# Optimization experiments

Hardware: AMD Instinct MI355X
Metric: run time of the kernel (lower is better)

The kernel has to match this reference:

```python
import jax, jax.numpy as jnp
import numpy as np

N, E, MUL, ATTR, NBASIS = 30000, 480000, 32, 8, 8
AVG_NEIGH = 16.0
INV_SQRT3 = 1.0 / np.sqrt(3.0).astype(np.float32)  # wigner 3j (1,1,0)
LOG2 = float(np.log(2.0))


def ssp(x):
    # shifted softplus: softplus(x) - log(2)
    return jax.nn.softplus(x) - LOG2


def setup_inputs() -> dict:
    key = jax.random.key(0)
    ks = jax.random.split(key, 15)
    return {
        "node_s": jax.random.normal(ks[0], (N, MUL), jnp.float32),
        "node_v": jax.random.normal(ks[1], (N, MUL, 3), jnp.float32),
        "node_attr": jax.random.uniform(ks[2], (N, ATTR), jnp.float32),
        "edge_attr": jax.random.normal(ks[3], (E, 4), jnp.float32),       # [sh0 | sh1(3)]
        "edge_scalars": jax.random.uniform(ks[4], (E, NBASIS), jnp.float32),
        "W1_0": jax.random.normal(ks[5], (MUL, MUL), jnp.float32),
        "W1_1": jax.random.normal(ks[6], (MUL, MUL), jnp.float32),
        "Wfc1": jax.random.normal(ks[7], (NBASIS, NBASIS), jnp.float32),
        "Wfc2": jax.random.normal(ks[8], (NBASIS, 4 * MUL), jnp.float32),
        "W2_0": jax.random.normal(ks[9], (2 * MUL, MUL), jnp.float32),
        "W2_1": jax.random.normal(ks[10], (2 * MUL, MUL), jnp.float32),
        "Wsc0": jax.random.normal(ks[11], (MUL, ATTR, MUL), jnp.float32),
        "Wsc1": jax.random.normal(ks[12], (MUL, ATTR, MUL), jnp.float32),
        "edge_src": jax.random.randint(ks[13], (E,), 0, N, jnp.int32),
        "edge_dst": jax.random.randint(ks[14], (E,), 0, N, jnp.int32),
    }


def reference(node_s, node_v, node_attr, edge_attr, edge_scalars,
              W1_0, W1_1, Wfc1, Wfc2, W2_0, W2_1, Wsc0, Wsc1,
              edge_src, edge_dst):
    n_nodes, mul = node_s.shape
    # --- fc: radial MLP -> per-edge TP weights (shared_weights=False) ---
    h = ssp(edge_scalars @ Wfc1 * (1.0 / np.sqrt(Wfc1.shape[0])))
    w = h @ Wfc2 * (1.0 / np.sqrt(Wfc2.shape[0]))                 # [E, 4*MUL]
    w00, w01, w10, w11 = jnp.split(w, 4, axis=1)                  # instruction order
    # --- lin1: per-irrep linear (fan-in normalized) ---
    inv_m = 1.0 / np.sqrt(mul)
    x0 = node_s @ W1_0 * inv_m                                    # [N, MUL]
    x1 = jnp.einsum('nud,uw->nwd', node_v, W1_1) * inv_m          # [N, MUL, 3]
    # --- gather destination-node features per edge ---
    x0d, x1d = x0[edge_dst], x1[edge_dst]
    sh0, sh1 = edge_attr[:, :1], edge_attr[:, 1:4]
    # --- uvu tensor product with per-edge weights ---
    s_a = w00 * x0d * sh0                                         # 0e x 0e -> 0e
    s_b = w11 * jnp.einsum('eud,ed->eu', x1d, sh1) * INV_SQRT3    # 1o x 1o -> 0e
    v_a = (w01 * x0d)[:, :, None] * sh1[:, None, :]               # 0e x 1o -> 1o
    v_b = w10[:, :, None] * x1d * sh0[:, :, None]                 # 1o x 0e -> 1o
    mid_s = jnp.concatenate([s_a, s_b], axis=1)                   # [E, 64]  (64x0e)
    mid_v = jnp.concatenate([v_a, v_b], axis=1)                   # [E, 64, 3] (64x1o)
    # --- scatter-sum over edge_src, normalized by sqrt(avg_num_neighbors) ---
    inv_nb = 1.0 / np.sqrt(AVG_NEIGH)
    agg_s = jax.ops.segment_sum(mid_s, edge_src, num_segments=n_nodes) * inv_nb
    agg_v = jax.ops.segment_sum(mid_v, edge_src, num_segments=n_nodes) * inv_nb
    # --- lin2 ---
    inv_2m = 1.0 / np.sqrt(2.0 * mul)
    out0 = agg_s @ W2_0 * inv_2m                                  # [N, MUL]
    out1 = jnp.einsum('nud,uw->nwd', agg_v, W2_1) * inv_2m        # [N, MUL, 3]
    # --- self-connection: fully-connected TP (attr is scalar 8x0e) ---
    sc_norm = 1.0 / np.sqrt(mul * node_attr.shape[1])
    sc0 = jnp.einsum('nu,nv,uvw->nw', node_s, node_attr, Wsc0) * sc_norm
    sc1 = jnp.einsum('nud,nv,uvw->nwd', node_v, node_attr, Wsc1) * sc_norm
    o0 = out0 + sc0
    o1 = out1 + sc1
    return jnp.concatenate([o0, o1.reshape(n_nodes, mul * 3)], axis=1)  # [N, 128]
```

## Files before the change

### kernel.cpp

```cpp
#include <hip/hip_runtime.h>
#include <math.h>

#define N_NODES 30000
#define N_EDGES 480000

typedef __attribute__((ext_vector_type(8))) short short8;
typedef __attribute__((ext_vector_type(4))) float f32x4;
typedef __attribute__((ext_vector_type(2))) float f32x2;

__device__ __forceinline__ unsigned short f2bf(float f) {
    unsigned u = __float_as_uint(f);
    u += 0x7fff + ((u >> 16) & 1);
    return (unsigned short)(u >> 16);
}
__device__ __forceinline__ float bfLO(unsigned v) { return __uint_as_float(v << 16); }
__device__ __forceinline__ float bfHI(unsigned v) { return __uint_as_float(v & 0xffff0000u); }
__device__ __forceinline__ unsigned packbf(float a, float b) {
    return (unsigned)f2bf(a) | ((unsigned)f2bf(b) << 16);
}
__device__ __forceinline__ unsigned ptk(float a, float b) {
    return (__float_as_uint(a) >> 16) | (__float_as_uint(b) & 0xffff0000u);
}

union U8 { short8 v; unsigned u[4]; };
union C4 { f32x4 v; float f[4]; };

__global__ __launch_bounds__(256) void k_pre(
    const float* __restrict__ node_s,
    const float* __restrict__ node_v,
    const float* __restrict__ W1_0,
    const float* __restrict__ W1_1,
    const float* __restrict__ Wsc0,
    const float* __restrict__ Wsc1,
    const float* __restrict__ W2_0,
    const float* __restrict__ W2_1,
    const int* __restrict__ edge_src,
    int* __restrict__ deg,
    unsigned short* __restrict__ xnode,
    unsigned* __restrict__ bsc0,
    unsigned* __restrict__ bsc1,
    unsigned* __restrict__ b20,
    unsigned* __restrict__ b21)
{
    __shared__ float sVT[16 * 100];
    __shared__ float sXo[16 * 140];
    int tid = threadIdx.x;

    if (blockIdx.x >= 1875) {
        int b = blockIdx.x - 1875;
        const float* Wm = (b == 0) ? Wsc0 : (b == 1) ? Wsc1 : (b == 2) ? W2_0 : W2_1;
        unsigned* dst = (b == 0) ? bsc0 : (b == 1) ? bsc1 : (b == 2) ? b20 : b21;
        float scale = (b < 2) ? 0.0625f : 0.03125f;
        int nu = (b < 2) ? 4096 : 1024;
        for (int idx = tid; idx < nu; idx += 256) {
            int jp = idx & 3;
            int lane = (idx >> 2) & 63;
            int ft = (idx >> 8) & 1;
            int kc = idx >> 9;
            int quad = lane >> 4, col = lane & 15;
            int k = kc * 32 + quad * 8 + jp * 2;
            int c = ft * 16 + col;
            dst[idx] = packbf(Wm[k * 32 + c] * scale, Wm[(k + 1) * 32 + c] * scale);
        }
        return;
    }

    atomicAdd(&deg[edge_src[blockIdx.x * 256 + tid]], 1);

    int nbase = blockIdx.x * 16;
    for (int i = tid; i < 1536; i += 256) {
        int nl = i / 96, r = i - nl * 96;
        int u = r / 3, d = r - u * 3;
        sVT[nl * 100 + d * 32 + u] = node_v[(size_t)nbase * 96 + i];
    }
    __syncthreads();

    int lane = tid & 63;
    int wv = tid >> 6;
    int col = lane & 15, quad = lane >> 4, m = lane & 15;

    const float* W1 = (wv == 0) ? W1_0 : W1_1;
    U8 bf0, bf1;
#pragma unroll
    for (int p = 0; p < 4; ++p) {
        int k = quad * 8 + 2 * p;
        bf0.u[p] = packbf(W1[k * 32 + col],      W1[(k + 1) * 32 + col]);
        bf1.u[p] = packbf(W1[k * 32 + col + 16], W1[(k + 1) * 32 + col + 16]);
    }

    U8 af;
    if (wv == 0) {
        const float* sp = node_s + (size_t)(nbase + m) * 32 + quad * 8;
        float4 a0 = *(const float4*)(sp);
        float4 a1 = *(const float4*)(sp + 4);
        af.u[0] = packbf(a0.x, a0.y); af.u[1] = packbf(a0.z, a0.w);
        af.u[2] = packbf(a1.x, a1.y); af.u[3] = packbf(a1.z, a1.w);
    } else {
        int R = 16 * (wv - 1) + m;
        int nl = R / 3, d = R - nl * 3;
        const float* vp = sVT + nl * 100 + d * 32 + quad * 8;
        af.u[0] = packbf(vp[0], vp[1]); af.u[1] = packbf(vp[2], vp[3]);
        af.u[2] = packbf(vp[4], vp[5]); af.u[3] = packbf(vp[6], vp[7]);
    }

    f32x4 acc0 = {0.f, 0.f, 0.f, 0.f};
    f32x4 acc1 = {0.f, 0.f, 0.f, 0.f};
    acc0 = __builtin_amdgcn_mfma_f32_16x16x32_bf16(af.v, bf0.v, acc0, 0, 0, 0);
    acc1 = __builtin_amdgcn_mfma_f32_16x16x32_bf16(af.v, bf1.v, acc1, 0, 0, 0);

    C4 c0, c1;
    c0.v = acc0; c1.v = acc1;
    if (wv == 0) {
#pragma unroll
        for (int r = 0; r < 4; ++r) {
            int nl = (quad << 2) + r;
            sXo[nl * 140 + col]      = c0.f[r];
            sXo[nl * 140 + col + 16] = c1.f[r];
        }
    } else {
#pragma unroll
        for (int r = 0; r < 4; ++r) {
            int R = 16 * (wv - 1) + (quad << 2) + r;
            int nl = R / 3, d = R - nl * 3;
            sXo[nl * 140 + (1 + d) * 34 + col]      = c0.f[r];
            sXo[nl * 140 + (1 + d) * 34 + col + 16] = c1.f[r];
        }
    }
    __syncthreads();

    const float inv_m = 0.1767766953f;
    for (int i = tid; i < 512; i += 256) {
        int nl = i >> 5, u = i & 31;
        const float* xp = sXo + nl * 140;
        uint2 pk;
        pk.x = packbf(xp[u] * inv_m,       xp[34 + u] * inv_m);
        pk.y = packbf(xp[68 + u] * inv_m,  xp[102 + u] * inv_m);
        *(uint2*)(xnode + (size_t)(nbase + nl) * 128 + u * 4) = pk;
    }
}

__global__ __launch_bounds__(1024) void scan_kernel(const int* __restrict__ deg,
                                                    int* __restrict__ offs,
                                                    int* __restrict__ cursor) {
    __shared__ int sdeg[N_NODES];
    __shared__ int wsum[16];
    int tid = threadIdx.x;
#pragma unroll
    for (int k = 0; k < 30; ++k) {
        int idx = k * 1024 + tid;
        if (idx < N_NODES) sdeg[idx] = deg[idx];
    }
    __syncthreads();
    int base = tid * 30;
    int s = 0;
    if (base < N_NODES) {
#pragma unroll
        for (int k = 0; k < 30; ++k) s += sdeg[base + k];
    }
    int lane = tid & 63, wid = tid >> 6;
    int inc = s;
#pragma unroll
    for (int d = 1; d < 64; d <<= 1) {
        int o = __shfl_up(inc, d, 64);
        if (lane >= d) inc += o;
    }
    if (lane == 63) wsum[wid] = inc;
    __syncthreads();
    if (tid < 16) {
        int v = wsum[tid];
        int t = v;
#pragma unroll
        for (int d = 1; d < 16; d <<= 1) {
            int o = __shfl_up(t, d, 64);
            if (tid >= d) t += o;
        }
        wsum[tid] = t - v;
    }
    __syncthreads();
    int run = inc - s + wsum[wid];
    if (base < N_NODES) {
#pragma unroll
        for (int k = 0; k < 30; ++k) {
            int n = base + k;
            int d = sdeg[n];
            sdeg[n] = run;
            run += d;
        }
    }
    __syncthreads();
#pragma unroll
    for (int k = 0; k < 30; ++k) {
        int idx = k * 1024 + tid;
        if (idx < N_NODES) {
            int v = sdeg[idx];
            offs[idx] = v;
            cursor[idx] = v;
        }
    }
    if (tid == 0) offs[N_NODES] = N_EDGES;
}

__global__ __launch_bounds__(256) void fill_kernel(
    const float* __restrict__ edge_attr,
    const float* __restrict__ edge_scalars,
    const float* __restrict__ Wfc1,
    const int* __restrict__ edge_src,
    const int* __restrict__ edge_dst,
    int* __restrict__ cursor,
    uint4* __restrict__ rec)
{
    __shared__ float sW[64];
    int tid = threadIdx.x;
    if (tid < 64) sW[tid] = Wfc1[tid];
    __syncthreads();

    int e = blockIdx.x * 256 + tid;
    float4 es0 = *(const float4*)(edge_scalars + (size_t)e * 8);
    float4 es1 = *(const float4*)(edge_scalars + (size_t)e * 8 + 4);
    float4 ea  = *(const float4*)(edge_attr + (size_t)e * 4);
    int src = edge_src[e];
    int dst = edge_dst[e];
    int pos = atomicAdd(&cursor[src], 1);

    const float inv8 = 0.3535533906f;
    float h[8];
#pragma unroll
    for (int i = 0; i < 8; ++i) {
        float acc = es0.x * sW[0 * 8 + i];
        acc = fmaf(es0.y, sW[1 * 8 + i], acc);
        acc = fmaf(es0.z, sW[2 * 8 + i], acc);
        acc = fmaf(es0.w, sW[3 * 8 + i], acc);
        acc = fmaf(es1.x, sW[4 * 8 + i], acc);
        acc = fmaf(es1.y, sW[5 * 8 + i], acc);
        acc = fmaf(es1.z, sW[6 * 8 + i], acc);
        acc = fmaf(es1.w, sW[7 * 8 + i], acc);
        acc *= inv8;
        float ax = fabsf(acc);
        float tt = __expf(-ax);
        h[i] = fmaxf(acc, 0.f) + __logf(1.f + tt) - 0.6931471806f;
    }
    uint4 r0, r1;
    r0.x = packbf(h[0], h[1]); r0.y = packbf(h[2], h[3]);
    r0.z = packbf(h[4], h[5]); r0.w = packbf(h[6], h[7]);
    r1.x = packbf(ea.x, ea.y); r1.y = packbf(ea.z, ea.w);
    r1.z = ((unsigned)dst) << 8;
    r1.w = 0;
    rec[2 * pos]     = r0;
    rec[2 * pos + 1] = r1;
}

struct GAcc {
    float sa, sb, va2, vb2;
    f32x2 va01, vb01;
};

__device__ __forceinline__ void gstep(
    uint4& RS0, uint4& RS1, uint2& XS, const uint4& RN1, uint2& XN,
    int& t, int cntH, int& pf, int L,
    const char* recc, const char* xbc,
    const f32x2* wfA, const f32x2* wfB, GAcc& g)
{
    float hv[8];
    hv[0] = bfLO(RS0.x); hv[1] = bfHI(RS0.x);
    hv[2] = bfLO(RS0.y); hv[3] = bfHI(RS0.y);
    hv[4] = bfLO(RS0.z); hv[5] = bfHI(RS0.z);
    hv[6] = bfLO(RS0.w); hv[7] = bfHI(RS0.w);
    float sh0  = bfLO(RS1.x), s1xe = bfHI(RS1.x);
    float s1ye = bfLO(RS1.y), s1ze = bfHI(RS1.y);
    float xv0 = bfLO(XS.x), xd0 = bfHI(XS.x);
    float xd1 = bfLO(XS.y), xd2 = bfHI(XS.y);
    bool ok = (t < cntH);

    RS0 = *(const uint4*)(recc + pf);
    RS1 = *(const uint4*)(recc + pf + 16);
    pf = min(pf + 64, L);
    XN = *(const uint2*)(xbc + RN1.z);

    f32x2 aA = {0.f, 0.f}, aB = {0.f, 0.f};
#pragma unroll
    for (int q = 0; q < 8; ++q) {
        f32x2 hh = {hv[q], hv[q]};
        aA = __builtin_elementwise_fma(hh, wfA[q], aA);
        aB = __builtin_elementwise_fma(hh, wfB[q], aB);
    }
    float a00 = ok ? aA.x : 0.f;
    float a01 = ok ? aA.y : 0.f;
    float a10 = ok ? aB.x : 0.f;
    float a11 = ok ? aB.y : 0.f;

    float dot = xd0 * s1xe + xd1 * s1ye + xd2 * s1ze;
    g.sa = fmaf(a00 * sh0, xv0, g.sa);
    g.sb = fmaf(a11, dot, g.sb);
    float w01x0 = a01 * xv0;
    float t10 = a10 * sh0;
    f32x2 wb = {w01x0, w01x0};
    f32x2 tb = {t10, t10};
    f32x2 s01 = {s1xe, s1ye};
    f32x2 xd01 = {xd0, xd1};
    g.va01 = __builtin_elementwise_fma(wb, s01, g.va01);
    g.vb01 = __builtin_elementwise_fma(tb, xd01, g.vb01);
    g.va2 = fmaf(w01x0, s1ze, g.va2);
    g.vb2 = fmaf(t10, xd2, g.vb2);
    ++t;
}

__global__ __launch_bounds__(256) void k_main(
    const int* __restrict__ offs,
    const uint4* __restrict__ rec,
    const float* __restrict__ Wfc2,
    const unsigned short* __restrict__ xnode,
    const float* __restrict__ node_s,
    const float* __restrict__ node_v,
    const float* __restrict__ node_attr,
    const unsigned* __restrict__ bsc0,
    const unsigned* __restrict__ bsc1,
    const unsigned* __restrict__ b20,
    const unsigned* __restrict__ b21,
    float* __restrict__ out)
{
    __shared__ float sWf[1024];
    __shared__ float sS[16 * 33];
    __shared__ float sV[16 * 100];
    __shared__ unsigned short sAgg[16 * 264];
    int tid = threadIdx.x;

    const float inv8 = 0.3535533906f;
    const float inv_s3 = 0.5773502692f;
    for (int i = tid; i < 1024; i += 256) {
        float sc = ((i & 127) >= 96) ? inv8 * inv_s3 : inv8;
        sWf[i] = Wfc2[i] * sc;
    }
    int nbase = blockIdx.x * 16;
    for (int i = tid; i < 512; i += 256)
        sS[(i >> 5) * 33 + (i & 31)] = node_s[(size_t)nbase * 32 + i];
    for (int i = tid; i < 1536; i += 256)
        sV[(i / 96) * 100 + (i % 96)] = node_v[(size_t)nbase * 96 + i];
    __syncthreads();

    int lane = tid & 63;
    int u = lane & 31;
    int half = lane >> 5;
    int wv = tid >> 6;

    f32x2 wfA[8], wfB[8];
#pragma unroll
    for (int q = 0; q < 8; ++q) {
        const float* wp = sWf + q * 128 + u;
        wfA[q].x = wp[0];  wfA[q].y = wp[32];
        wfB[q].x = wp[64]; wfB[q].y = wp[96];
    }

    int nfirst = nbase + wv * 4;
    int beg = offs[nfirst];
#pragma unroll 1
    for (int j = 0; j < 4; ++j) {
        int end = offs[nfirst + j + 1];
        int cnt = end - beg;

        GAcc g;
        g.sa = 0.f; g.sb = 0.f; g.va2 = 0.f; g.vb2 = 0.f;
        g.va01 = (f32x2){0.f, 0.f};
        g.vb01 = (f32x2){0.f, 0.f};

        if (cnt > 0) {
            const char* recc = (const char*)rec;
            const char* xbc  = (const char*)xnode + u * 8;
            int T = (cnt + 1) >> 1;
            int cntH = (cnt + 1 - half) >> 1;
            int L = (end - 1) * 32;
            int b0 = (beg + half) * 32;

            uint4 r00, r01, r10, r11, r20, r21, r30, r31, r40, r41, r50, r51;
            uint2 x0, x1, x2, x3, x4, x5;
            x4.x = 0u; x4.y = 0u; x5.x = 0u; x5.y = 0u;
            int p;
            p = min(b0,       L); r00 = *(const uint4*)(recc + p); r01 = *(const uint4*)(recc + p + 16);
            p = min(b0 + 64,  L); r10 = *(const uint4*)(recc + p); r11 = *(const uint4*)(recc + p + 16);
            p = min(b0 + 128, L); r20 = *(const uint4*)(recc + p); r21 = *(const uint4*)(recc + p + 16);
            p = min(b0 + 192, L); r30 = *(const uint4*)(recc + p); r31 = *(const uint4*)(recc + p + 16);
            p = min(b0 + 256, L); r40 = *(const uint4*)(recc + p); r41 = *(const uint4*)(recc + p + 16);
            p = min(b0 + 320, L); r50 = *(const uint4*)(recc + p); r51 = *(const uint4*)(recc + p + 16);
            int pf = min(b0 + 384, L);
            x0 = *(const uint2*)(xbc + r01.z);
            x1 = *(const uint2*)(xbc + r11.z);
            x2 = *(const uint2*)(xbc + r21.z);
            x3 = *(const uint2*)(xbc + r31.z);

            int t = 0;
            int Tm = T - 5;
            while (t < Tm) {
                gstep(r00, r01, x0, r41, x4, t, cntH, pf, L, recc, xbc, wfA, wfB, g);
                gstep(r10, r11, x1, r51, x5, t, cntH, pf, L, recc, xbc, wfA, wfB, g);
                gstep(r20, r21, x2, r01, x0, t, cntH, pf, L, recc, xbc, wfA, wfB, g);
                gstep(r30, r31, x3, r11, x1, t, cntH, pf, L, recc, xbc, wfA, wfB, g);
                gstep(r40, r41, x4, r21, x2, t, cntH, pf, L, recc, xbc, wfA, wfB, g);
                gstep(r50, r51, x5, r31, x3, t, cntH, pf, L, recc, xbc, wfA, wfB, g);
            }
            if (t < T) gstep(r00, r01, x0, r41, x4, t, cntH, pf, L, recc, xbc, wfA, wfB, g);
            if (t < T) gstep(r10, r11, x1, r51, x5, t, cntH, pf, L, recc, xbc, wfA, wfB, g);
            if (t < T) gstep(r20, r21, x2, r01, x0, t, cntH, pf, L, recc, xbc, wfA, wfB, g);
            if (t < T) gstep(r30, r31, x3, r11, x1, t, cntH, pf, L, recc, xbc, wfA, wfB, g);
            if (t < T) gstep(r40, r41, x4, r21, x2, t, cntH, pf, L, recc, xbc, wfA, wfB, g);
        }

        g.sa      += __shfl_xor(g.sa, 32, 64);
        g.sb      += __shfl_xor(g.sb, 32, 64);
        g.va01.x  += __shfl_xor(g.va01.x, 32, 64);
        g.va01.y  += __shfl_xor(g.va01.y, 32, 64);
        g.vb01.x  += __shfl_xor(g.vb01.x, 32, 64);
        g.vb01.y  += __shfl_xor(g.vb01.y, 32, 64);
        g.va2     += __shfl_xor(g.va2, 32, 64);
        g.vb2     += __shfl_xor(g.vb2, 32, 64);

        int nl = wv * 4 + j;
        unsigned short* ap = sAgg + nl * 264;
        if (half == 0) {
            ap[u]       = f2bf(g.sa);
            ap[32 + u]  = f2bf(g.sb);
            ap[64 + u]  = f2bf(g.va01.x);
            ap[96 + u]  = f2bf(g.vb01.x);
        } else {
            ap[128 + u] = f2bf(g.va01.y);
            ap[160 + u] = f2bf(g.vb01.y);
            ap[192 + u] = f2bf(g.va2);
            ap[224 + u] = f2bf(g.vb2);
        }
        beg = end;
    }
    __syncthreads();

    int col = lane & 15;
    int quad = lane >> 4;
    int m = col;
    bool is_s = (wv == 0);
    int sub = wv - 1;

    const short* Bs = (const short*)(is_s ? bsc0 : bsc1);
    const short* B2 = (const short*)(is_s ? b20 : b21);

    int aBase, fbase, fstep, n_a;
    if (is_s) {
        aBase = m * 264;
        fbase = m * 33;
        fstep = 1;
        n_a = nbase + m;
    } else {
        int r16 = 16 * sub + m;
        int nl = r16 / 3;
        int dd = r16 - nl * 3;
        aBase = nl * 264 + 64 + 64 * dd;
        fbase = nl * 100 + dd;
        fstep = 3;
        n_a = nbase + nl;
    }
    float4 A0 = *(const float4*)(node_attr + (size_t)n_a * 8);
    float4 A1 = *(const float4*)(node_attr + (size_t)n_a * 8 + 4);
    float aa0 = A0.x, aa1 = A0.y, aa2 = A0.z, aa3 = A0.w;
    float aa4 = A1.x, aa5 = A1.y, aa6 = A1.z, aa7 = A1.w;

    f32x4 acc0 = {0.f, 0.f, 0.f, 0.f};
    f32x4 acc1 = {0.f, 0.f, 0.f, 0.f};

#pragma unroll
    for (int kc = 0; kc < 2; ++kc) {
        short8 af = *(const short8*)((const short*)sAgg + aBase + kc * 32 + quad * 8);
        short8 bf0 = *(const short8*)(B2 + ((kc * 2 + 0) * 64 + lane) * 8);
        short8 bf1 = *(const short8*)(B2 + ((kc * 2 + 1) * 64 + lane) * 8);
        acc0 = __builtin_amdgcn_mfma_f32_16x16x32_bf16(af, bf0, acc0, 0, 0, 0);
        acc1 = __builtin_amdgcn_mfma_f32_16x16x32_bf16(af, bf1, acc1, 0, 0, 0);
    }
    const float* Sf = is_s ? sS : sV;
#pragma unroll
    for (int kc = 0; kc < 8; ++kc) {
        int uu = kc * 4 + quad;
        float f = Sf[fbase + uu * fstep];
        U8 af;
        af.u[0] = ptk(f * aa0, f * aa1);
        af.u[1] = ptk(f * aa2, f * aa3);
        af.u[2] = ptk(f * aa4, f * aa5);
        af.u[3] = ptk(f * aa6, f * aa7);
        short8 bf0 = *(const short8*)(Bs + ((kc * 2 + 0) * 64 + lane) * 8);
        short8 bf1 = *(const short8*)(Bs + ((kc * 2 + 1) * 64 + lane) * 8);
        acc0 = __builtin_amdgcn_mfma_f32_16x16x32_bf16(af.v, bf0, acc0, 0, 0, 0);
        acc1 = __builtin_amdgcn_mfma_f32_16x16x32_bf16(af.v, bf1, acc1, 0, 0, 0);
    }

    C4 c0, c1;
    c0.v = acc0; c1.v = acc1;
    if (is_s) {
#pragma unroll
        for (int r = 0; r < 4; ++r) {
            int n = nbase + (quad << 2) + r;
            out[(size_t)n * 128 + col]      = c0.f[r];
            out[(size_t)n * 128 + col + 16] = c1.f[r];
        }
    } else {
#pragma unroll
        for (int r = 0; r < 4; ++r) {
            int rl = 16 * sub + (quad << 2) + r;
            int nn = rl / 3;
            int dd = rl - nn * 3;
            int n = nbase + nn;
            out[(size_t)n * 128 + 32 + 3 * col + dd]        = c0.f[r];
            out[(size_t)n * 128 + 32 + 3 * (col + 16) + dd] = c1.f[r];
        }
    }
}

extern "C" void kernel_launch(void* const* d_in, const int* in_sizes, int n_in,
                              void* d_out, int out_size, void* d_ws, size_t ws_size,
                              hipStream_t stream) {
    const float* node_s       = (const float*)d_in[0];
    const float* node_v       = (const float*)d_in[1];
    const float* node_attr    = (const float*)d_in[2];
    const float* edge_attr    = (const float*)d_in[3];
    const float* edge_scalars = (const float*)d_in[4];
    const float* W1_0 = (const float*)d_in[5];
    const float* W1_1 = (const float*)d_in[6];
    const float* Wfc1 = (const float*)d_in[7];
    const float* Wfc2 = (const float*)d_in[8];
    const float* W2_0 = (const float*)d_in[9];
    const float* W2_1 = (const float*)d_in[10];
    const float* Wsc0 = (const float*)d_in[11];
    const float* Wsc1 = (const float*)d_in[12];
    const int* edge_src = (const int*)d_in[13];
    const int* edge_dst = (const int*)d_in[14];

    char* ws = (char*)d_ws;
    unsigned short* xnode = (unsigned short*)(ws);
    uint4* rec            = (uint4*)(ws + 7680000);
    int* deg    = (int*)(ws + 23040000);
    int* offs   = (int*)(ws + 23160000);
    int* cursor = (int*)(ws + 23280016);
    unsigned* bsc0 = (unsigned*)(ws + 23400064);
    unsigned* bsc1 = (unsigned*)(ws + 23416448);
    unsigned* b20  = (unsigned*)(ws + 23432832);
    unsigned* b21  = (unsigned*)(ws + 23436928);

    hipMemsetAsync(deg, 0, (size_t)N_NODES * sizeof(int), stream);
    k_pre<<<1879, 256, 0, stream>>>(node_s, node_v, W1_0, W1_1, Wsc0, Wsc1,
                                    W2_0, W2_1, edge_src, deg, xnode,
                                    bsc0, bsc1, b20, b21);
    scan_kernel<<<1, 1024, 0, stream>>>(deg, offs, cursor);
    fill_kernel<<<1875, 256, 0, stream>>>(edge_attr, edge_scalars, Wfc1,
                                          edge_src, edge_dst, cursor, rec);
    k_main<<<1875, 256, 0, stream>>>(offs, rec, Wfc2, xnode,
                                     node_s, node_v, node_attr,
                                     bsc0, bsc1, b20, b21, (float*)d_out);
}
```

Before: 230.2 us.

## Record per-edge slot in counting pass and fold scan into preprocessing kernel

A new counting kernel stores each edge's atomic return value, so the fill kernel computes its position as offs[src]+epos instead of issuing a second atomic. The single-block scan kernel is removed, and block 0 of k_pre now performs a chunked prefix scan that runs alongside the node transforms. k_main reads Wfc2 straight into registers instead of staging it through shared memory, which drops a barrier. In exchange this adds one launch, uses the output buffer as scratch for epos, and makes block 0 of k_pre a serial scan that may become the critical path.

```diff
diff --git a/kernel.cpp b/kernel.cpp
--- a/kernel.cpp
+++ b/kernel.cpp
@@ -24,6 +24,15 @@
 
 union U8 { short8 v; unsigned u[4]; };
 union C4 { f32x4 v; float f[4]; };
+
+__global__ __launch_bounds__(256) void k_count(
+    const int* __restrict__ edge_src,
+    int* __restrict__ deg,
+    int* __restrict__ epos)
+{
+    int e = blockIdx.x * 256 + threadIdx.x;
+    epos[e] = atomicAdd(&deg[edge_src[e]], 1);
+}
 
 __global__ __launch_bounds__(256) void k_pre(
     const float* __restrict__ node_s,
@@ -34,20 +43,69 @@
     const float* __restrict__ Wsc1,
     const float* __restrict__ W2_0,
     const float* __restrict__ W2_1,
-    const int* __restrict__ edge_src,
-    int* __restrict__ deg,
+    const int* __restrict__ deg,
+    int* __restrict__ offs,
     unsigned short* __restrict__ xnode,
     unsigned* __restrict__ bsc0,
     unsigned* __restrict__ bsc1,
     unsigned* __restrict__ b20,
     unsigned* __restrict__ b21)
 {
-    __shared__ float sVT[16 * 100];
-    __shared__ float sXo[16 * 140];
+    __shared__ __align__(16) char smem[15360];
+    __shared__ int wsb[6];
+    float* sVT = (float*)smem;
+    float* sXo = (float*)(smem + 6400);
+    int*   sdg = (int*)smem;
     int tid = threadIdx.x;
 
-    if (blockIdx.x >= 1875) {
-        int b = blockIdx.x - 1875;
+    if (blockIdx.x == 0) {
+        int lane = tid & 63, wid = tid >> 6;
+        int running = 0;
+        for (int c = 0; c < N_NODES; c += 3840) {
+            int size = min(3840, N_NODES - c);
+#pragma unroll
+            for (int k = 0; k < 15; ++k) {
+                int i = tid + k * 256;
+                sdg[i] = (i < size) ? deg[c + i] : 0;
+            }
+            __syncthreads();
+            int bt = tid * 15;
+            int s = 0;
+#pragma unroll
+            for (int k = 0; k < 15; ++k) s += sdg[bt + k];
+            int inc = s;
+#pragma unroll
+            for (int d = 1; d < 64; d <<= 1) {
+                int o = __shfl_up(inc, d, 64);
+                if (lane >= d) inc += o;
+            }
+            if (lane == 63) wsb[wid] = inc;
+            __syncthreads();
+            if (tid == 0) {
+                int t0 = 0;
+#pragma unroll
+                for (int w = 0; w < 4; ++w) { int v = wsb[w]; wsb[w] = t0; t0 += v; }
+                wsb[4] = t0;
+            }
+            __syncthreads();
+            int run2 = inc - s + wsb[wid] + running;
+#pragma unroll
+            for (int k = 0; k < 15; ++k) {
+                int idx = bt + k;
+                int gi = c + idx;
+                int d = sdg[idx];
+                if (gi < N_NODES) offs[gi] = run2;
+                run2 += d;
+            }
+            running += wsb[4];
+            __syncthreads();
+        }
+        if (tid == 0) offs[N_NODES] = N_EDGES;
+        return;
+    }
+
+    if (blockIdx.x >= 1876) {
+        int b = blockIdx.x - 1876;
         const float* Wm = (b == 0) ? Wsc0 : (b == 1) ? Wsc1 : (b == 2) ? W2_0 : W2_1;
         unsigned* dst = (b == 0) ? bsc0 : (b == 1) ? bsc1 : (b == 2) ? b20 : b21;
         float scale = (b < 2) ? 0.0625f : 0.03125f;
@@ -65,9 +123,7 @@
         return;
     }
 
-    atomicAdd(&deg[edge_src[blockIdx.x * 256 + tid]], 1);
-
-    int nbase = blockIdx.x * 16;
+    int nbase = (blockIdx.x - 1) * 16;
     for (int i = tid; i < 1536; i += 256) {
         int nl = i / 96, r = i - nl * 96;
         int u = r / 3, d = r - u * 3;
@@ -139,74 +195,14 @@
     }
 }
 
-__global__ __launch_bounds__(1024) void scan_kernel(const int* __restrict__ deg,
-                                                    int* __restrict__ offs,
-                                                    int* __restrict__ cursor) {
-    __shared__ int sdeg[N_NODES];
-    __shared__ int wsum[16];
-    int tid = threadIdx.x;
-#pragma unroll
-    for (int k = 0; k < 30; ++k) {
-        int idx = k * 1024 + tid;
-        if (idx < N_NODES) sdeg[idx] = deg[idx];
-    }
-    __syncthreads();
-    int base = tid * 30;
-    int s = 0;
-    if (base < N_NODES) {
-#pragma unroll
-        for (int k = 0; k < 30; ++k) s += sdeg[base + k];
-    }
-    int lane = tid & 63, wid = tid >> 6;
-    int inc = s;
-#pragma unroll
-    for (int d = 1; d < 64; d <<= 1) {
-        int o = __shfl_up(inc, d, 64);
-        if (lane >= d) inc += o;
-    }
-    if (lane == 63) wsum[wid] = inc;
-    __syncthreads();
-    if (tid < 16) {
-        int v = wsum[tid];
-        int t = v;
-#pragma unroll
-        for (int d = 1; d < 16; d <<= 1) {
-            int o = __shfl_up(t, d, 64);
-            if (tid >= d) t += o;
-        }
-        wsum[tid] = t - v;
-    }
-    __syncthreads();
-    int run = inc - s + wsum[wid];
-    if (base < N_NODES) {
-#pragma unroll
-        for (int k = 0; k < 30; ++k) {
-            int n = base + k;
-            int d = sdeg[n];
-            sdeg[n] = run;
-            run += d;
-        }
-    }
-    __syncthreads();
-#pragma unroll
-    for (int k = 0; k < 30; ++k) {
-        int idx = k * 1024 + tid;
-        if (idx < N_NODES) {
-            int v = sdeg[idx];
-            offs[idx] = v;
-            cursor[idx] = v;
-        }
-    }
-    if (tid == 0) offs[N_NODES] = N_EDGES;
-}
-
 __global__ __launch_bounds__(256) void fill_kernel(
     const float* __restrict__ edge_attr,
     const float* __restrict__ edge_scalars,
     const float* __restrict__ Wfc1,
     const int* __restrict__ edge_src,
     const int* __restrict__ edge_dst,
-    int* __restrict__ cursor,
+    const int* __restrict__ offs,
+    const int* __restrict__ epos,
     uint4* __restrict__ rec)
 {
     __shared__ float sW[64];
@@ -220,7 +216,7 @@
     float4 ea  = *(const float4*)(edge_attr + (size_t)e * 4);
     int src = edge_src[e];
     int dst = edge_dst[e];
-    int pos = atomicAdd(&cursor[src], 1);
+    int pos = offs[src] + epos[e];
 
     const float inv8 = 0.3535533906f;
     float h[8];
@@ -318,36 +314,32 @@
     const unsigned* __restrict__ b21,
     float* __restrict__ out)
 {
-    __shared__ float sWf[1024];
     __shared__ float sS[16 * 33];
     __shared__ float sV[16 * 100];
     __shared__ unsigned short sAgg[16 * 264];
     int tid = threadIdx.x;
 
-    const float inv8 = 0.3535533906f;
-    const float inv_s3 = 0.5773502692f;
-    for (int i = tid; i < 1024; i += 256) {
-        float sc = ((i & 127) >= 96) ? inv8 * inv_s3 : inv8;
-        sWf[i] = Wfc2[i] * sc;
-    }
     int nbase = blockIdx.x * 16;
     for (int i = tid; i < 512; i += 256)
         sS[(i >> 5) * 33 + (i & 31)] = node_s[(size_t)nbase * 32 + i];
     for (int i = tid; i < 1536; i += 256)
         sV[(i / 96) * 100 + (i % 96)] = node_v[(size_t)nbase * 96 + i];
-    __syncthreads();
 
     int lane = tid & 63;
     int u = lane & 31;
     int half = lane >> 5;
     int wv = tid >> 6;
 
+    const float inv8 = 0.3535533906f;
+    const float i8s3 = 0.3535533906f * 0.5773502692f;
     f32x2 wfA[8], wfB[8];
 #pragma unroll
     for (int q = 0; q < 8; ++q) {
-        const float* wp = sWf + q * 128 + u;
-        wfA[q].x = wp[0];  wfA[q].y = wp[32];
-        wfB[q].x = wp[64]; wfB[q].y = wp[96];
+        const float* wp = Wfc2 + q * 128 + u;
+        wfA[q].x = wp[0]  * inv8;
+        wfA[q].y = wp[32] * inv8;
+        wfB[q].x = wp[64] * inv8;
+        wfB[q].y = wp[96] * i8s3;
     }
 
     int nfirst = nbase + wv * 4;
@@ -531,19 +523,20 @@
     uint4* rec            = (uint4*)(ws + 7680000);
     int* deg    = (int*)(ws + 23040000);
     int* offs   = (int*)(ws + 23160000);
-    int* cursor = (int*)(ws + 23280016);
     unsigned* bsc0 = (unsigned*)(ws + 23400064);
     unsigned* bsc1 = (unsigned*)(ws + 23416448);
     unsigned* b20  = (unsigned*)(ws + 23432832);
     unsigned* b21  = (unsigned*)(ws + 23436928);
 
+    int* epos = (int*)d_out;
+
     hipMemsetAsync(deg, 0, (size_t)N_NODES * sizeof(int), stream);
-    k_pre<<<1879, 256, 0, stream>>>(node_s, node_v, W1_0, W1_1, Wsc0, Wsc1,
-                                    W2_0, W2_1, edge_src, deg, xnode,
+    k_count<<<1875, 256, 0, stream>>>(edge_src, deg, epos);
+    k_pre<<<1880, 256, 0, stream>>>(node_s, node_v, W1_0, W1_1, Wsc0, Wsc1,
+                                    W2_0, W2_1, deg, offs, xnode,
                                     bsc0, bsc1, b20, b21);
-    scan_kernel<<<1, 1024, 0, stream>>>(deg, offs, cursor);
     fill_kernel<<<1875, 256, 0, stream>>>(edge_attr, edge_scalars, Wfc1,
-                                          edge_src, edge_dst, cursor, rec);
+                                          edge_src, edge_dst, offs, epos, rec);
     k_main<<<1875, 256, 0, stream>>>(offs, rec, Wfc2, xnode,
                                      node_s, node_v, node_attr,
                                      bsc0, bsc1, b20, b21, (float*)d_out);
```

Measured after the change: 250.6 us. 8.9% more time.
